# Kernel tuning notes

Measured on AMD Instinct MI355X. Metric: run time of the kernel, lower is better.

Reference implementation:

```python
import jax, jax.numpy as jnp
import numpy as np

B, C, D, H, W = 8, 96, 8, 32, 32
HW, DIM, NH = H * W, C * D, 4
DH = DIM // NH
EPS_NORM = 1e-12
EPS_LN = 1e-5


def setup_inputs() -> dict:
    key = jax.random.key(0)
    ks = jax.random.split(key, 10)
    s = 0.02
    return {
        "x": jax.random.normal(ks[0], (B, C, D, H, W), jnp.float32),
        "pos_embed": jax.random.normal(ks[1], (1, HW, DIM), jnp.float32) * s,
        "qkv_w": jax.random.normal(ks[2], (3 * DIM, DIM), jnp.float32) * s,
        "proj_w": jax.random.normal(ks[3], (DIM, DIM), jnp.float32) * s,
        "proj_b": jnp.zeros((DIM,), jnp.float32),
        "temperature": jnp.ones((NH, 1, 1), jnp.float32),
        "ln_gamma": jnp.ones((DIM,), jnp.float32),
        "ln_beta": jnp.zeros((DIM,), jnp.float32),
        "dw_w": jax.random.normal(ks[4], (C, 1, 3, 3, 3), jnp.float32) * s,
        "dw_b": jnp.zeros((C,), jnp.float32),
        "pw_w": jax.random.normal(ks[5], (C, C, 1, 1, 1), jnp.float32) * s,
        "pw_b": jnp.zeros((C,), jnp.float32),
    }


def _l2norm_seq(t):
    # normalize over the HW axis (dim=-2), matching F.normalize(dim=-2)
    n = jnp.sqrt(jnp.sum(t * t, axis=-2, keepdims=True))
    return t / jnp.maximum(n, EPS_NORM)


def _dsconv(y, dw_w, dw_b, pw_w, pw_b):
    dn = ("NCDHW", "OIDHW", "NCDHW")
    z = jax.lax.conv_general_dilated(y, dw_w, (1, 1, 1), [(1, 1)] * 3,
                                     dimension_numbers=dn, feature_group_count=C)
    z = z + dw_b[None, :, None, None, None]
    z = jax.lax.conv_general_dilated(z, pw_w, (1, 1, 1), [(0, 0)] * 3,
                                     dimension_numbers=dn)
    return z + pw_b[None, :, None, None, None]


def reference(x, pos_embed, qkv_w, proj_w, proj_b, temperature,
              ln_gamma, ln_beta, dw_w, dw_b, pw_w, pw_b):
    save = x
    # b c d h w -> b (h w) (c d)
    t = jnp.transpose(x, (0, 3, 4, 1, 2)).reshape(B, HW, DIM)
    t = t + pos_embed
    # qkv projection (no bias)
    qkv = (t @ qkv_w.T).reshape(B, HW, 3, NH, DH)
    qkv = jnp.transpose(qkv, (2, 0, 3, 1, 4))  # [3,B,NH,HW,DH]
    q, k, v = qkv[0], qkv[1], qkv[2]
    q = _l2norm_seq(q)
    k = _l2norm_seq(k)
    attn = jnp.einsum("bhnd,bhmd->bhnm", q, k) * temperature  # temp broadcasts [NH,1,1]
    attn = jax.nn.softmax(attn, axis=-1)  # dropout = identity at eval
    o = jnp.einsum("bhnm,bhmd->bhnd", attn, v)
    o = jnp.transpose(o, (0, 2, 1, 3)).reshape(B, HW, DIM)
    o = o @ proj_w.T + proj_b
    # LayerNorm applied to attention output
    mu = jnp.mean(o, axis=-1, keepdims=True)
    var = jnp.mean((o - mu) ** 2, axis=-1, keepdims=True)
    o = (o - mu) / jnp.sqrt(var + EPS_LN) * ln_gamma + ln_beta
    # b (h w) (c d) -> b c d h w
    o = o.reshape(B, H, W, C, D)
    o = jnp.transpose(o, (0, 3, 4, 1, 2))
    y = o + save
    return y + _dsconv(y, dw_w, dw_b, pw_w, pw_b)
```

## Files before the change

### kernel.cpp

```cpp
#include <hip/hip_runtime.h>

typedef unsigned short u16;
typedef unsigned int u32;

typedef __attribute__((ext_vector_type(8))) short short8;
typedef __attribute__((ext_vector_type(4))) float floatx4;

__device__ __forceinline__ float bf2f(u16 u) { return __uint_as_float(((u32)u) << 16); }
__device__ __forceinline__ u16 f2bf(float f) {
    u32 x = __float_as_uint(f);
    x += 0x7fffu + ((x >> 16) & 1u);
    return (u16)(x >> 16);
}
__device__ __forceinline__ void gl_lds16(const void* g, void* l) {
    __builtin_amdgcn_global_load_lds((const __attribute__((address_space(1))) u32*)g,
                                     (__attribute__((address_space(3))) u32*)l, 16, 0, 0);
}


__global__ __launch_bounds__(256) void k_tpos(const float* __restrict__ x,
                                              const float* __restrict__ pos,
                                              u16* __restrict__ t) {
    __shared__ float tile[64][65];
    const int b = blockIdx.z, hw0 = blockIdx.y * 64, cd0 = blockIdx.x * 64;
    const int tid = threadIdx.x;
#pragma unroll
    for (int i = 0; i < 16; i++) {
        int f = i * 256 + tid;
        int cdl = f >> 6, hwl = f & 63;
        int cd = cd0 + cdl, c = cd >> 3, d = cd & 7;
        tile[cdl][hwl] = x[(size_t)(((b * 96 + c) * 8 + d)) * 1024 + hw0 + hwl];
    }
    __syncthreads();
#pragma unroll
    for (int it = 0; it < 2; it++) {
        int u = it * 256 + tid;
        int ch = u >> 6, l = u & 63;
        int n16l = ch >> 1, kcl = ch & 1;
        int hwl = n16l * 16 + (l & 15);
        int cdl = kcl * 32 + (l >> 4) * 8;
        int row = b * 1024 + hw0 + hwl;
        int cd = cd0 + cdl;
        const float* pp = pos + (size_t)(hw0 + hwl) * 768 + cd;
        float4 p0 = *(const float4*)pp;
        float4 p1 = *(const float4*)(pp + 4);
        short8 v;
        v[0] = (short)f2bf(tile[cdl + 0][hwl] + p0.x);
        v[1] = (short)f2bf(tile[cdl + 1][hwl] + p0.y);
        v[2] = (short)f2bf(tile[cdl + 2][hwl] + p0.z);
        v[3] = (short)f2bf(tile[cdl + 3][hwl] + p0.w);
        v[4] = (short)f2bf(tile[cdl + 4][hwl] + p1.x);
        v[5] = (short)f2bf(tile[cdl + 5][hwl] + p1.y);
        v[6] = (short)f2bf(tile[cdl + 6][hwl] + p1.z);
        v[7] = (short)f2bf(tile[cdl + 7][hwl] + p1.w);
        size_t chunk = (size_t)(row >> 4) * 24 + (cd >> 5);
        *(short8*)(t + chunk * 512 + l * 8) = v;
    }
}

__global__ __launch_bounds__(256) void k_cvt(const float* __restrict__ wq,
                                             const float* __restrict__ wp,
                                             const float* __restrict__ wpw,
                                             u16* __restrict__ out) {
    const int NQ = 144 * 24 * 64;
    const int NP = NQ + 48 * 24 * 64;
    int u = blockIdx.x * 256 + threadIdx.x;
    if (u < NP) {
        const float* w = (u < NQ) ? wq : wp;
        int ub = (u < NQ) ? u : u - NQ;
        int chunk = ub >> 6, l = ub & 63;
        int n16 = chunk / 24, kc = chunk - n16 * 24;
        int n = n16 * 16 + (l & 15);
        int k0 = kc * 32 + (l >> 4) * 8;
        const float* src = w + (size_t)n * 768 + k0;
        float4 a = *(const float4*)src;
        float4 b2 = *(const float4*)(src + 4);
        short8 v;
        v[0] = (short)f2bf(a.x);  v[1] = (short)f2bf(a.y);
        v[2] = (short)f2bf(a.z);  v[3] = (short)f2bf(a.w);
        v[4] = (short)f2bf(b2.x); v[5] = (short)f2bf(b2.y);
        v[6] = (short)f2bf(b2.z); v[7] = (short)f2bf(b2.w);
        *(short8*)(out + (size_t)u * 8) = v;
    } else {
        int i = u - NP;
        out[(size_t)NP * 8 + i] = f2bf(wpw[i]);
    }
}

template <int MODE>
__global__ __launch_bounds__(256) void gemm_bt(const u16* __restrict__ A,
                                               const u16* __restrict__ Bw,
                                               int M, int N, int K,
                                               u16* __restrict__ qo, u16* __restrict__ ko,
                                               u16* __restrict__ vo,
                                               const float* __restrict__ bias,
                                               float* __restrict__ Co) {
    __shared__ __align__(16) u16 lAB[32 * 512];
    u16* lA = lAB;
    u16* lB = lAB + 16 * 512;
    const int tid = threadIdx.x;
    const int lane = tid & 63;
    const int wv = tid >> 6;
    const int wr = wv >> 1, wc = wv & 1;
    const int ntiles = N >> 7;
    const int mtiles = M >> 7;
    const int lin = blockIdx.x;
    const int xcd = lin & 7;
    const int idx = lin >> 3;
    const int mlocal = idx / ntiles;
    const int ntile = idx - mlocal * ntiles;
    const int m0 = (xcd * (mtiles >> 3) + mlocal) << 7;
    const int n0 = ntile << 7;
    const int lr = lane & 15;
    const int lq = lane >> 4;

    floatx4 acc[4][4];
#pragma unroll
    for (int i = 0; i < 4; i++)
#pragma unroll
        for (int j = 0; j < 4; j++) acc[i][j] = (floatx4){0.f, 0.f, 0.f, 0.f};

    const int m16 = m0 >> 4, n16 = n0 >> 4;
    for (int kc2 = 0; kc2 < (K >> 6); kc2++) {
        __syncthreads();
#pragma unroll
        for (int kh = 0; kh < 2; kh++) {
#pragma unroll
            for (int i = 0; i < 2; i++) {
                int ch16 = i * 4 + wv;
                int kc = kc2 * 2 + kh;
                const u16* ga = A + ((size_t)(m16 + ch16) * 24 + kc) * 512 + lane * 8;
                gl_lds16(ga, (char*)lA + (kh * 8 + ch16) * 1024);
                const u16* gb = Bw + ((size_t)(n16 + ch16) * 24 + kc) * 512 + lane * 8;
                gl_lds16(gb, (char*)lB + (kh * 8 + ch16) * 1024);
            }
        }
        __syncthreads();
#pragma unroll
        for (int kh = 0; kh < 2; kh++) {
            short8 af[4], bfr[4];
#pragma unroll
            for (int tt = 0; tt < 4; tt++) {
                af[tt] = *(const short8*)(lA + ((kh * 8 + wr * 4 + tt) * 64 + lane) * 8);
                bfr[tt] = *(const short8*)(lB + ((kh * 8 + wc * 4 + tt) * 64 + lane) * 8);
            }
#pragma unroll
            for (int mt = 0; mt < 4; mt++)
#pragma unroll
                for (int nt = 0; nt < 4; nt++)
                    acc[mt][nt] = __builtin_amdgcn_mfma_f32_16x16x32_bf16(af[mt], bfr[nt], acc[mt][nt], 0, 0, 0);
        }
    }

    if (MODE == 0) {
        const int region = n0 / 768;
        const int n0r = n0 - region * 768;
        if (region == 0) {
#pragma unroll
            for (int nt = 0; nt < 4; nt++) {
                int colb = n0r + wc * 64 + nt * 16;
                int h = colb / 192;
                int dh = colb - h * 192 + lr;
#pragma unroll
                for (int mt = 0; mt < 4; mt++) {
#pragma unroll
                    for (int r = 0; r < 4; r++) {
                        int row = m0 + wr * 64 + mt * 16 + lq * 4 + r;
                        int b = row >> 10, n = row & 1023;
                        qo[((size_t)(b * 4 + h) * 1024 + n) * 192 + dh] = f2bf(acc[mt][nt][r]);
                    }
                }
            }
        } else {
            __syncthreads();
            if (region == 1) {
#pragma unroll
                for (int nt = 0; nt < 4; nt++) {
                    int lch = wc * 2 + (nt >> 1);
                    int offbase = (((nt & 1) * 2 + (lr >> 3)) * 16) * 8 + (lr & 7);
#pragma unroll
                    for (int mt = 0; mt < 4; mt++) {
                        u16* cp2 = lAB + (((wr * 4 + mt) * 4 + lch) * 512);
#pragma unroll
                        for (int r = 0; r < 4; r++)
                            cp2[offbase + (lq * 4 + r) * 8] = f2bf(acc[mt][nt][r]);
                    }
                }
            } else {
#pragma unroll
                for (int nt = 0; nt < 4; nt++) {
#pragma unroll
                    for (int mt = 0; mt < 4; mt++) {
                        u16* cp2 = lAB + (((wr * 2 + (mt >> 1)) * 8 + wc * 4 + nt) * 512);
                        int ob = (((mt & 1) * 2 + (lq >> 1)) * 16 + lr) * 8 + (lq & 1) * 4;
#pragma unroll
                        for (int r = 0; r < 4; r++)
                            cp2[ob + r] = f2bf(acc[mt][nt][r]);
                    }
                }
            }
            __syncthreads();
            const int b = m0 >> 10;
            const int ml = m0 & 1023;
#pragma unroll
            for (int i = 0; i < 8; i++) {
                int ci = wv * 8 + i;
                short8 val = *(const short8*)(lAB + ci * 512 + lane * 8);
                if (region == 1) {
                    int a = ci >> 2, bb = ci & 3;
                    int cg = n0r + bb * 32;
                    int h = cg / 192;
                    int dh32 = (cg - h * 192) >> 5;
                    size_t gaddr = (size_t)(b * 4 + h) * 196608 +
                                   (size_t)((((ml >> 4) + a) * 6 + dh32)) * 512 + lane * 8;
                    *(short8*)(ko + gaddr) = val;
                } else {
                    int a = ci >> 3, bb = ci & 7;
                    int cg = n0r + bb * 16;
                    int h = cg / 192;
                    int dh16 = (cg - h * 192) >> 4;
                    size_t gaddr = (size_t)(b * 4 + h) * 196608 +
                                   (size_t)((((ml >> 5) + a) * 12 + dh16)) * 512 + lane * 8;
                    *(short8*)(vo + gaddr) = val;
                }
            }
        }
    } else {
#pragma unroll
        for (int nt = 0; nt < 4; nt++) {
            int col = n0 + wc * 64 + nt * 16 + lr;
            float bv = bias[col];
#pragma unroll
            for (int mt = 0; mt < 4; mt++) {
#pragma unroll
                for (int r = 0; r < 4; r++) {
                    int row = m0 + wr * 64 + mt * 16 + lq * 4 + r;
                    Co[(size_t)row * N + col] = acc[mt][nt][r] + bv;
                }
            }
        }
    }
}

__global__ void k_sq(const u16* __restrict__ q, const u16* __restrict__ k,
                     float* __restrict__ sqq, float* __restrict__ sqk) {
    int bh = blockIdx.x;
    int part = blockIdx.y;
    int dh = threadIdx.x;
    const u16* qp = q + ((size_t)bh * 1024 + part * 128) * 192 + dh;
    float aq = 0.f;
#pragma unroll 4
    for (int n = 0; n < 128; n++) {
        float a = bf2f(qp[(size_t)n * 192]);
        aq += a * a;
    }
    const u16* kbase = k + (size_t)bh * 196608 + (dh >> 5) * 512 + ((dh >> 3) & 3) * 128 + (dh & 7);
    float ak = 0.f;
#pragma unroll 4
    for (int n = 0; n < 128; n++) {
        int nn = part * 128 + n;
        float c2 = bf2f(kbase[(nn >> 4) * 3072 + (nn & 15) * 8]);
        ak += c2 * c2;
    }
    atomicAdd(&sqq[bh * 192 + dh], aq);
    atomicAdd(&sqk[bh * 192 + dh], ak);
}

__global__ void k_scale(const float* __restrict__ sqq, const float* __restrict__ sqk,
                        const float* __restrict__ temp, float* __restrict__ cs) {
    int bh = blockIdx.x;
    int dh = threadIdx.x;
    float rq = 1.f / fmaxf(sqrtf(sqq[bh * 192 + dh]), 1e-12f);
    float rk = 1.f / fmaxf(sqrtf(sqk[bh * 192 + dh]), 1e-12f);
    cs[bh * 192 + dh] = rq * rk * temp[bh & 3];
}

__global__ __launch_bounds__(128) void k_attn(const u16* __restrict__ q,
                                              const u16* __restrict__ kmat,
                                              const u16* __restrict__ vT,
                                              const float* __restrict__ cs,
                                              u16* __restrict__ o) {
    __shared__ __align__(16) u16 lK[24 * 512];
    __shared__ __align__(16) u16 lV[24 * 512];
    __shared__ __align__(16) u16 lP[2 * 2048];
    const int lin = blockIdx.x;
    const int qb = (lin >> 3) & 15;
    const int bh = (lin & 7) * 4 + (lin >> 7);
    const int b = bh >> 2, h = bh & 3;
    const int tid = threadIdx.x;
    const int lane = tid & 63;
    const int wv = tid >> 6;
    const int lr = lane & 15;
    const int lq = lane >> 4;
    const int koff = lq * 8;

    const u16* qbase = q + (size_t)bh * 1024 * 192;
    const u16* kbase = kmat + (size_t)bh * 196608;
    const u16* vbase = vT + (size_t)bh * 196608;
    const float* cp = cs + bh * 192;

    short8 qf[2][6];
#pragma unroll
    for (int t = 0; t < 2; t++) {
        const int qrow = qb * 64 + wv * 32 + t * 16 + lr;
        const u16* qp = qbase + (size_t)qrow * 192;
#pragma unroll
        for (int ks = 0; ks < 6; ks++) {
            short8 raw = *(const short8*)(qp + ks * 32 + koff);
            short8 sc;
#pragma unroll
            for (int j = 0; j < 8; j++) {
                float f = bf2f((u16)raw[j]) * cp[ks * 32 + koff + j];
                sc[j] = (short)f2bf(f);
            }
            qf[t][ks] = sc;
        }
    }

    float l_r[2][4];
    floatx4 oacc[2][12];
#pragma unroll
    for (int t = 0; t < 2; t++) {
#pragma unroll
        for (int r = 0; r < 4; r++) l_r[t][r] = 0.f;
#pragma unroll
        for (int vt = 0; vt < 12; vt++) oacc[t][vt] = (floatx4){0.f, 0.f, 0.f, 0.f};
    }

    u16* lp = lP + wv * 2048;

    for (int kb = 0; kb < 16; kb++) {
        __syncthreads();
#pragma unroll
        for (int i = 0; i < 12; i++) {
            int ch = i * 2 + wv;
            int ks = ch >> 2, nt = ch & 3;
            const u16* gk = kbase + ((size_t)(kb * 4 + nt) * 6 + ks) * 512 + lane * 8;
            gl_lds16(gk, (char*)lK + ch * 1024);
            int ks2 = ch / 12, vt2 = ch - ks2 * 12;
            const u16* gv = vbase + ((size_t)(kb * 2 + ks2) * 12 + vt2) * 512 + lane * 8;
            gl_lds16(gv, (char*)lV + ch * 1024);
        }
        __syncthreads();

        floatx4 s0[4], s1[4];
#pragma unroll
        for (int nt = 0; nt < 4; nt++) {
            s0[nt] = (floatx4){0.f, 0.f, 0.f, 0.f};
            s1[nt] = (floatx4){0.f, 0.f, 0.f, 0.f};
        }
#pragma unroll
        for (int ks = 0; ks < 6; ks++) {
#pragma unroll
            for (int nt = 0; nt < 4; nt++) {
                short8 kf = *(const short8*)(lK + ((ks * 4 + nt) * 64 + lane) * 8);
                s0[nt] = __builtin_amdgcn_mfma_f32_16x16x32_bf16(qf[0][ks], kf, s0[nt], 0, 0, 0);
                s1[nt] = __builtin_amdgcn_mfma_f32_16x16x32_bf16(qf[1][ks], kf, s1[nt], 0, 0, 0);
            }
        }

        float rs0[4] = {0.f, 0.f, 0.f, 0.f}, rs1[4] = {0.f, 0.f, 0.f, 0.f};
#pragma unroll
        for (int nt = 0; nt < 4; nt++)
#pragma unroll
            for (int r = 0; r < 4; r++) {
                float p0 = __expf(s0[nt][r]);
                s0[nt][r] = p0;
                rs0[r] += p0;
                float p1 = __expf(s1[nt][r]);
                s1[nt][r] = p1;
                rs1[r] += p1;
            }
#pragma unroll
        for (int m = 1; m < 16; m <<= 1)
#pragma unroll
            for (int r = 0; r < 4; r++) {
                rs0[r] += __shfl_xor(rs0[r], m);
                rs1[r] += __shfl_xor(rs1[r], m);
            }
#pragma unroll
        for (int r = 0; r < 4; r++) {
            l_r[0][r] += rs0[r];
            l_r[1][r] += rs1[r];
        }
#pragma unroll
        for (int nt = 0; nt < 4; nt++) {
            int base2 = (nt >> 1) * 512 + ((nt & 1) * 2 + (lr >> 3)) * 128 + (lr & 7);
#pragma unroll
            for (int r = 0; r < 4; r++) {
                lp[base2 + (lq * 4 + r) * 8] = f2bf(s0[nt][r]);
                lp[1024 + base2 + (lq * 4 + r) * 8] = f2bf(s1[nt][r]);
            }
        }

#pragma unroll
        for (int ks2 = 0; ks2 < 2; ks2++) {
            short8 pf0 = *(const short8*)(lp + ks2 * 512 + lane * 8);
            short8 pf1 = *(const short8*)(lp + 1024 + ks2 * 512 + lane * 8);
#pragma unroll
            for (int vt = 0; vt < 12; vt++) {
                short8 vf = *(const short8*)(lV + ((ks2 * 12 + vt) * 64 + lane) * 8);
                oacc[0][vt] = __builtin_amdgcn_mfma_f32_16x16x32_bf16(pf0, vf, oacc[0][vt], 0, 0, 0);
                oacc[1][vt] = __builtin_amdgcn_mfma_f32_16x16x32_bf16(pf1, vf, oacc[1][vt], 0, 0, 0);
            }
        }
    }

#pragma unroll
    for (int t = 0; t < 2; t++) {
        float inv[4];
#pragma unroll
        for (int r = 0; r < 4; r++) inv[r] = 1.f / l_r[t][r];
#pragma unroll
        for (int vt = 0; vt < 12; vt++) {
            int col = h * 192 + vt * 16 + lr;
#pragma unroll
            for (int r = 0; r < 4; r++) {
                int rowg = b * 1024 + qb * 64 + wv * 32 + t * 16 + lq * 4 + r;
                size_t addr = (size_t)(rowg >> 4) * 12288 + (col >> 5) * 512 +
                              ((col >> 3) & 3) * 128 + (rowg & 15) * 8 + (col & 7);
                o[addr] = f2bf(oacc[t][vt][r] * inv[r]);
            }
        }
    }
}

__global__ __launch_bounds__(256) void k_lnstats(const float* __restrict__ o2,
                                                 float* __restrict__ mu,
                                                 float* __restrict__ rstd) {
    int row = blockIdx.x;
    int tid = threadIdx.x;
    const float* p = o2 + (size_t)row * 768;
    float s = 0.f, ss = 0.f;
    for (int i = tid; i < 768; i += 256) {
        float v = p[i];
        s += v;
        ss += v * v;
    }
#pragma unroll
    for (int m = 32; m >= 1; m >>= 1) {
        s += __shfl_xor(s, m);
        ss += __shfl_xor(ss, m);
    }
    __shared__ float as[4], ass[4];
    if ((tid & 63) == 0) {
        as[tid >> 6] = s;
        ass[tid >> 6] = ss;
    }
    __syncthreads();
    if (tid == 0) {
        float S = as[0] + as[1] + as[2] + as[3];
        float SS = ass[0] + ass[1] + ass[2] + ass[3];
        float m_ = S * (1.f / 768.f);
        float v = SS * (1.f / 768.f) - m_ * m_;
        v = fmaxf(v, 0.f);
        mu[row] = m_;
        rstd[row] = rsqrtf(v + 1e-5f);
    }
}

__global__ __launch_bounds__(256) void k_lnt(const float* __restrict__ o2,
                                             const float* __restrict__ mu,
                                             const float* __restrict__ rstd,
                                             const float* __restrict__ gamma,
                                             const float* __restrict__ beta,
                                             const float* __restrict__ x,
                                             float* __restrict__ y) {
    __shared__ float tile[64][65];
    const int b = blockIdx.z, hw0 = blockIdx.y * 64, cd0 = blockIdx.x * 64;
    const int tid = threadIdx.x;
#pragma unroll
    for (int i = 0; i < 16; i++) {
        int f = i * 256 + tid;
        int hwl = f >> 6, cdl = f & 63;
        int row = b * 1024 + hw0 + hwl;
        float v = o2[(size_t)row * 768 + cd0 + cdl];
        v = (v - mu[row]) * rstd[row] * gamma[cd0 + cdl] + beta[cd0 + cdl];
        tile[hwl][cdl] = v;
    }
    __syncthreads();
#pragma unroll
    for (int i = 0; i < 16; i++) {
        int f = i * 256 + tid;
        int cdl = f >> 6, hwl = f & 63;
        int cd = cd0 + cdl, c = cd >> 3, d = cd & 7;
        size_t addr = (size_t)((b * 96 + c) * 8 + d) * 1024 + hw0 + hwl;
        y[addr] = tile[hwl][cdl] + x[addr];
    }
}

__global__ __launch_bounds__(256) void k_dw(const float* __restrict__ y,
                                            const float* __restrict__ w,
                                            const float* __restrict__ bias,
                                            float* __restrict__ z) {
    __shared__ float ly[8192];
    const int bc = blockIdx.x;
    const int c = bc % 96;
    const int tid = threadIdx.x;
    const size_t base = (size_t)bc * 8192;

#pragma unroll
    for (int i = 0; i < 8; i++) {
        int i4 = i * 256 + tid;
        *(float4*)(ly + i4 * 4) = *(const float4*)(y + base + i4 * 4);
    }
    float wt[27];
#pragma unroll
    for (int j = 0; j < 27; j++) wt[j] = w[c * 27 + j];
    const float bv = bias[c];
    __syncthreads();

    const int wcol = tid & 31;
    const int hh = tid >> 5;

    for (int hb = 0; hb < 4; hb++) {
        const int h = hb * 8 + hh;
        float pl[3][9];
        auto loadplane = [&](int dd, float* p) {
#pragma unroll
            for (int kh = 0; kh < 3; kh++) {
                int h2 = h + kh - 1;
                bool hok = (unsigned)h2 < 32u;
                const float* row = ly + dd * 1024 + h2 * 32;
#pragma unroll
                for (int kw = 0; kw < 3; kw++) {
                    int w2 = wcol + kw - 1;
                    bool ok = hok && (unsigned)w2 < 32u;
                    p[kh * 3 + kw] = ok ? row[w2] : 0.f;
                }
            }
        };
#pragma unroll
        for (int j = 0; j < 9; j++) pl[0][j] = 0.f;
        loadplane(0, pl[1]);
#pragma unroll
        for (int d = 0; d < 8; d++) {
            if (d < 7) loadplane(d + 1, pl[2]);
            else {
#pragma unroll
                for (int j = 0; j < 9; j++) pl[2][j] = 0.f;
            }
            float acc = bv;
#pragma unroll
            for (int kd = 0; kd < 3; kd++)
#pragma unroll
                for (int j = 0; j < 9; j++) acc += wt[kd * 9 + j] * pl[kd][j];
            z[base + d * 1024 + h * 32 + wcol] = acc;
#pragma unroll
            for (int j = 0; j < 9; j++) { pl[0][j] = pl[1][j]; pl[1][j] = pl[2][j]; }
        }
    }
}

__global__ __launch_bounds__(256) void k_pw(const float* __restrict__ z,
                                            const u16* __restrict__ wbf,
                                            const float* __restrict__ bias,
                                            float* __restrict__ out) {
    __shared__ __align__(16) u16 lZ[128 * 104];
    __shared__ __align__(16) u16 lW[96 * 104];
    const int tid = threadIdx.x;
    const int lane = tid & 63;
    const int wv = tid >> 6;
    const int lr = lane & 15;
    const int lq = lane >> 4;
    const int koff = lq * 8;

    const int idx = blockIdx.x;
    const int q = idx & 7;
    const int bd = idx >> 3;
    const int b = bd >> 3, d = bd & 7;
    const int pos0 = q * 128;

    for (int i = tid; i < 96 * 96; i += 256) {
        int row = i / 96, col = i - row * 96;
        lW[row * 104 + col] = wbf[i];
    }
    {
        const int pos = tid & 127;
        const int cc0 = (tid >> 7) * 48;
        const size_t gbase = ((size_t)b * 96 * 8 + d) * 1024 + pos0 + pos;
#pragma unroll
        for (int g = 0; g < 6; g++) {
            short8 v;
#pragma unroll
            for (int j = 0; j < 8; j++) {
                int cc = cc0 + g * 8 + j;
                v[j] = (short)f2bf(z[gbase + (size_t)cc * 8192]);
            }
            *(short8*)(lZ + pos * 104 + cc0 + g * 8) = v;
        }
    }
    __syncthreads();

    floatx4 acc[6][2];
#pragma unroll
    for (int m = 0; m < 6; m++)
#pragma unroll
        for (int nt = 0; nt < 2; nt++) acc[m][nt] = (floatx4){0.f, 0.f, 0.f, 0.f};

#pragma unroll
    for (int ks = 0; ks < 3; ks++) {
        short8 bfrg[2];
#pragma unroll
        for (int nt = 0; nt < 2; nt++)
            bfrg[nt] = *(const short8*)(lZ + (wv * 32 + nt * 16 + lr) * 104 + ks * 32 + koff);
#pragma unroll
        for (int m = 0; m < 6; m++) {
            short8 afr = *(const short8*)(lW + (m * 16 + lr) * 104 + ks * 32 + koff);
#pragma unroll
            for (int nt = 0; nt < 2; nt++)
                acc[m][nt] = __builtin_amdgcn_mfma_f32_16x16x32_bf16(afr, bfrg[nt], acc[m][nt], 0, 0, 0);
        }
    }

#pragma unroll
    for (int m = 0; m < 6; m++) {
#pragma unroll
        for (int r = 0; r < 4; r++) {
            int c = m * 16 + lq * 4 + r;
            float bv = bias[c];
            size_t rowbase = ((size_t)(b * 96 + c) * 8 + d) * 1024 + pos0;
#pragma unroll
            for (int nt = 0; nt < 2; nt++) {
                int pos = wv * 32 + nt * 16 + lr;
                size_t a = rowbase + pos;
                out[a] = out[a] + bv + acc[m][nt][r];
            }
        }
    }
}

extern "C" void kernel_launch(void* const* d_in, const int* in_sizes, int n_in,
                              void* d_out, int out_size, void* d_ws, size_t ws_size,
                              hipStream_t stream) {
    (void)in_sizes; (void)n_in; (void)out_size; (void)ws_size;
    const float* x      = (const float*)d_in[0];
    const float* pos    = (const float*)d_in[1];
    const float* qkv_w  = (const float*)d_in[2];
    const float* proj_w = (const float*)d_in[3];
    const float* proj_b = (const float*)d_in[4];
    const float* temp   = (const float*)d_in[5];
    const float* ln_g   = (const float*)d_in[6];
    const float* ln_b   = (const float*)d_in[7];
    const float* dw_w   = (const float*)d_in[8];
    const float* dw_b   = (const float*)d_in[9];
    const float* pw_w   = (const float*)d_in[10];
    const float* pw_b   = (const float*)d_in[11];
    float* out = (float*)d_out;
    char* ws = (char*)d_ws;

    u16* t    = (u16*)(ws + 0);
    u16* vT   = (u16*)(ws + 12582912);
    u16* q    = (u16*)(ws + 25165824);
    u16* kk   = (u16*)(ws + 37748736);
    u16* wqb  = (u16*)(ws + 50331648);
    float* cs   = (float*)(ws + 55150592);
    float* sqq  = (float*)(ws + 55175168);
    float* sqk  = (float*)(ws + 55199744);
    float* mu   = (float*)(ws + 55224320);
    float* rstd = (float*)(ws + 55257088);
    u16* wpb  = wqb + 2304 * 768;
    u16* wpwb = wqb + 2304 * 768 + 768 * 768;
    u16* o   = t;
    float* o2 = (float*)q;
    float* z  = (float*)t;
    float* y  = out;

    k_tpos<<<dim3(12, 16, 8), 256, 0, stream>>>(x, pos, t);
    k_cvt<<<1188, 256, 0, stream>>>(qkv_w, proj_w, pw_w, wqb);
    gemm_bt<0><<<1152, 256, 0, stream>>>(t, wqb, 8192, 2304, 768, q, kk, vT, nullptr, nullptr);
    hipMemsetAsync(sqq, 0, 49152, stream);
    k_sq<<<dim3(32, 8), 192, 0, stream>>>(q, kk, sqq, sqk);
    k_scale<<<32, 192, 0, stream>>>(sqq, sqk, temp, cs);
    k_attn<<<512, 128, 0, stream>>>(q, kk, vT, cs, o);
    gemm_bt<1><<<384, 256, 0, stream>>>(o, wpb, 8192, 768, 768, nullptr, nullptr, nullptr, proj_b, o2);
    k_lnstats<<<8192, 256, 0, stream>>>(o2, mu, rstd);
    k_lnt<<<dim3(12, 16, 8), 256, 0, stream>>>(o2, mu, rstd, ln_g, ln_b, x, y);
    k_dw<<<768, 256, 0, stream>>>(y, dw_w, dw_b, z);
    k_pw<<<512, 256, 0, stream>>>(z, wpwb, pw_b, out);
}
```

Before: 288.8 us.

## Fuse q/k sum-of-squares and LayerNorm row stats into GEMM epilogues

```diff
diff --git a/kernel.cpp b/kernel.cpp
--- a/kernel.cpp
+++ b/kernel.cpp
@@ -94,7 +94,11 @@
                                                u16* __restrict__ qo, u16* __restrict__ ko,
                                                u16* __restrict__ vo,
                                                const float* __restrict__ bias,
-                                               float* __restrict__ Co) {
+                                               float* __restrict__ Co,
+                                               float* __restrict__ sqa,
+                                               float* __restrict__ ska,
+                                               float* __restrict__ musum,
+                                               float* __restrict__ sqsum) {
     __shared__ __align__(16) u16 lAB[32 * 512];
     u16* lA = lAB;
     u16* lB = lAB + 16 * 512;
@@ -155,6 +159,24 @@
     if (MODE == 0) {
         const int region = n0 / 768;
         const int n0r = n0 - region * 768;
+        const int bb0 = m0 >> 10;
+        if (region < 2) {
+            float* dst = (region == 0) ? sqa : ska;
+#pragma unroll
+            for (int nt = 0; nt < 4; nt++) {
+                int colb = n0r + wc * 64 + nt * 16;
+                int h = colb / 192;
+                int dh = colb - h * 192 + lr;
+                float s = 0.f;
+#pragma unroll
+                for (int mt = 0; mt < 4; mt++)
+#pragma unroll
+                    for (int r = 0; r < 4; r++) s += acc[mt][nt][r] * acc[mt][nt][r];
+                s += __shfl_xor(s, 16);
+                s += __shfl_xor(s, 32);
+                if (lq == 0) atomicAdd(&dst[(bb0 * 4 + h) * 192 + dh], s);
+            }
+        }
         if (region == 0) {
 #pragma unroll
             for (int nt = 0; nt < 4; nt++) {
@@ -226,44 +248,45 @@
             }
         }
     } else {
+        float bvv[4];
+#pragma unroll
+        for (int nt = 0; nt < 4; nt++) bvv[nt] = bias[n0 + wc * 64 + nt * 16 + lr];
 #pragma unroll
         for (int nt = 0; nt < 4; nt++) {
             int col = n0 + wc * 64 + nt * 16 + lr;
-            float bv = bias[col];
 #pragma unroll
             for (int mt = 0; mt < 4; mt++) {
 #pragma unroll
                 for (int r = 0; r < 4; r++) {
                     int row = m0 + wr * 64 + mt * 16 + lq * 4 + r;
-                    Co[(size_t)row * N + col] = acc[mt][nt][r] + bv;
-                }
-            }
-        }
-    }
-}
-
-__global__ void k_sq(const u16* __restrict__ q, const u16* __restrict__ k,
-                     float* __restrict__ sqq, float* __restrict__ sqk) {
-    int bh = blockIdx.x;
-    int part = blockIdx.y;
-    int dh = threadIdx.x;
-    const u16* qp = q + ((size_t)bh * 1024 + part * 128) * 192 + dh;
-    float aq = 0.f;
-#pragma unroll 4
-    for (int n = 0; n < 128; n++) {
-        float a = bf2f(qp[(size_t)n * 192]);
-        aq += a * a;
-    }
-    const u16* kbase = k + (size_t)bh * 196608 + (dh >> 5) * 512 + ((dh >> 3) & 3) * 128 + (dh & 7);
-    float ak = 0.f;
-#pragma unroll 4
-    for (int n = 0; n < 128; n++) {
-        int nn = part * 128 + n;
-        float c2 = bf2f(kbase[(nn >> 4) * 3072 + (nn & 15) * 8]);
-        ak += c2 * c2;
-    }
-    atomicAdd(&sqq[bh * 192 + dh], aq);
-    atomicAdd(&sqk[bh * 192 + dh], ak);
+                    Co[(size_t)row * N + col] = acc[mt][nt][r] + bvv[nt];
+                }
+            }
+        }
+#pragma unroll
+        for (int mt = 0; mt < 4; mt++) {
+#pragma unroll
+            for (int r = 0; r < 4; r++) {
+                float s = 0.f, ss = 0.f;
+#pragma unroll
+                for (int nt = 0; nt < 4; nt++) {
+                    float v = acc[mt][nt][r] + bvv[nt];
+                    s += v;
+                    ss += v * v;
+                }
+#pragma unroll
+                for (int m = 1; m < 16; m <<= 1) {
+                    s += __shfl_xor(s, m);
+                    ss += __shfl_xor(ss, m);
+                }
+                if (lr == 0) {
+                    int row = m0 + wr * 64 + mt * 16 + lq * 4 + r;
+                    atomicAdd(&musum[row], s);
+                    atomicAdd(&sqsum[row], ss);
+                }
+            }
+        }
+    }
 }
 
 __global__ void k_scale(const float* __restrict__ sqq, const float* __restrict__ sqk,
@@ -273,6 +296,18 @@
     float rq = 1.f / fmaxf(sqrtf(sqq[bh * 192 + dh]), 1e-12f);
     float rk = 1.f / fmaxf(sqrtf(sqk[bh * 192 + dh]), 1e-12f);
     cs[bh * 192 + dh] = rq * rk * temp[bh & 3];
+}
+
+__global__ __launch_bounds__(256) void k_lnfin(const float* __restrict__ musum,
+                                               const float* __restrict__ sqsum,
+                                               float* __restrict__ mu,
+                                               float* __restrict__ rstd) {
+    int row = blockIdx.x * 256 + threadIdx.x;
+    float m_ = musum[row] * (1.f / 768.f);
+    float v = sqsum[row] * (1.f / 768.f) - m_ * m_;
+    v = fmaxf(v, 0.f);
+    mu[row] = m_;
+    rstd[row] = rsqrtf(v + 1e-5f);
 }
 
 __global__ __launch_bounds__(128) void k_attn(const u16* __restrict__ q,
@@ -425,40 +460,6 @@
     }
 }
 
-__global__ __launch_bounds__(256) void k_lnstats(const float* __restrict__ o2,
-                                                 float* __restrict__ mu,
-                                                 float* __restrict__ rstd) {
-    int row = blockIdx.x;
-    int tid = threadIdx.x;
-    const float* p = o2 + (size_t)row * 768;
-    float s = 0.f, ss = 0.f;
-    for (int i = tid; i < 768; i += 256) {
-        float v = p[i];
-        s += v;
-        ss += v * v;
-    }
-#pragma unroll
-    for (int m = 32; m >= 1; m >>= 1) {
-        s += __shfl_xor(s, m);
-        ss += __shfl_xor(ss, m);
-    }
-    __shared__ float as[4], ass[4];
-    if ((tid & 63) == 0) {
-        as[tid >> 6] = s;
-        ass[tid >> 6] = ss;
-    }
-    __syncthreads();
-    if (tid == 0) {
-        float S = as[0] + as[1] + as[2] + as[3];
-        float SS = ass[0] + ass[1] + ass[2] + ass[3];
-        float m_ = S * (1.f / 768.f);
-        float v = SS * (1.f / 768.f) - m_ * m_;
-        v = fmaxf(v, 0.f);
-        mu[row] = m_;
-        rstd[row] = rsqrtf(v + 1e-5f);
-    }
-}
-
 __global__ __launch_bounds__(256) void k_lnt(const float* __restrict__ o2,
                                              const float* __restrict__ mu,
                                              const float* __restrict__ rstd,
@@ -654,11 +655,13 @@
     u16* q    = (u16*)(ws + 25165824);
     u16* kk   = (u16*)(ws + 37748736);
     u16* wqb  = (u16*)(ws + 50331648);
-    float* cs   = (float*)(ws + 55150592);
-    float* sqq  = (float*)(ws + 55175168);
-    float* sqk  = (float*)(ws + 55199744);
-    float* mu   = (float*)(ws + 55224320);
-    float* rstd = (float*)(ws + 55257088);
+    float* cs    = (float*)(ws + 55150592);
+    float* sqq   = (float*)(ws + 55175168);
+    float* sqk   = (float*)(ws + 55199744);
+    float* musum = (float*)(ws + 55224320);
+    float* sqsum = (float*)(ws + 55257088);
+    float* mu    = (float*)(ws + 55289856);
+    float* rstd  = (float*)(ws + 55322624);
     u16* wpb  = wqb + 2304 * 768;
     u16* wpwb = wqb + 2304 * 768 + 768 * 768;
     u16* o   = t;
@@ -668,13 +671,14 @@
 
     k_tpos<<<dim3(12, 16, 8), 256, 0, stream>>>(x, pos, t);
     k_cvt<<<1188, 256, 0, stream>>>(qkv_w, proj_w, pw_w, wqb);
-    gemm_bt<0><<<1152, 256, 0, stream>>>(t, wqb, 8192, 2304, 768, q, kk, vT, nullptr, nullptr);
-    hipMemsetAsync(sqq, 0, 49152, stream);
-    k_sq<<<dim3(32, 8), 192, 0, stream>>>(q, kk, sqq, sqk);
+    hipMemsetAsync(sqq, 0, 114688, stream);
+    gemm_bt<0><<<1152, 256, 0, stream>>>(t, wqb, 8192, 2304, 768, q, kk, vT, nullptr, nullptr,
+                                         sqq, sqk, nullptr, nullptr);
     k_scale<<<32, 192, 0, stream>>>(sqq, sqk, temp, cs);
     k_attn<<<512, 128, 0, stream>>>(q, kk, vT, cs, o);
-    gemm_bt<1><<<384, 256, 0, stream>>>(o, wpb, 8192, 768, 768, nullptr, nullptr, nullptr, proj_b, o2);
-    k_lnstats<<<8192, 256, 0, stream>>>(o2, mu, rstd);
+    gemm_bt<1><<<384, 256, 0, stream>>>(o, wpb, 8192, 768, 768, nullptr, nullptr, nullptr, proj_b,
+                                        o2, nullptr, nullptr, musum, sqsum);
+    k_lnfin<<<32, 256, 0, stream>>>(musum, sqsum, mu, rstd);
     k_lnt<<<dim3(12, 16, 8), 256, 0, stream>>>(o2, mu, rstd, ln_g, ln_b, x, y);
     k_dw<<<768, 256, 0, stream>>>(y, dw_w, dw_b, z);
     k_pw<<<512, 256, 0, stream>>>(z, wpwb, pw_b, out);
```

Result: faster. 276.3 us (-4.3%).
